# Kernel optimization log

Measured on AMD Instinct MI355X. Metric: run time of the kernel, lower is better.

Reference implementation:

```python
import jax, jax.numpy as jnp
import numpy as np

T, H, E, I, K = 4096, 1024, 16, 768, 8  # tokens, hidden, experts, intermediate, top_k


def setup_inputs() -> dict:
    key = jax.random.key(0)
    k0, k1, k2, k3, k4 = jax.random.split(key, 5)
    scale = 0.02
    return {
        "hidden_states": jax.random.normal(k0, (T, H), dtype=jnp.float32),
        "gate_w": jax.random.normal(k1, (H, E), dtype=jnp.float32) * scale,
        "w1": jax.random.normal(k2, (E, H, I), dtype=jnp.float32) * scale,  # gate proj
        "w3": jax.random.normal(k3, (E, H, I), dtype=jnp.float32) * scale,  # up proj
        "w2": jax.random.normal(k4, (E, I, H), dtype=jnp.float32) * scale,  # down proj
    }


def reference(hidden_states, gate_w, w1, w3, w2):
    x = hidden_states  # [T, H]
    # Router: replicated linear (no bias) -> softmax -> top-k -> renormalize
    router_logits = x @ gate_w  # [T, E]
    probs = jax.nn.softmax(router_logits.astype(jnp.float32), axis=-1)
    topk_w, topk_idx = jax.lax.top_k(probs, K)  # [T, K]
    topk_w = topk_w / jnp.sum(topk_w, axis=-1, keepdims=True)  # norm_topk_prob=True
    # Dense routing-weight matrix [T, E]: zero for non-selected experts
    dense_w = jnp.zeros((T, E), dtype=x.dtype)
    dense_w = dense_w.at[jnp.arange(T)[:, None], topk_idx].set(topk_w.astype(x.dtype))
    # SwiGLU experts, computed densely over experts and masked by routing weights
    h = jnp.einsum("th,ehi->tei", x, w1)  # [T, E, I]
    u = jnp.einsum("th,ehi->tei", x, w3)  # [T, E, I]
    act = jax.nn.silu(h) * u  # [T, E, I]
    out = jnp.einsum("tei,eih,te->th", act, w2, dense_w)  # weighted combine -> [T, H]
    return out
```

## Files before the change

kernel.cpp:

```cpp
#include <hip/hip_runtime.h>
#include <hip/hip_bf16.h>

#define T_ 4096
#define H_ 1024
#define E_ 16
#define I_ 768
#define KTOP 8
#define MAXSLOT 4096
#define ACT_ROWS 34816

typedef __attribute__((ext_vector_type(8))) short bf16x8;
typedef __attribute__((ext_vector_type(4))) float f32x4;

__device__ __forceinline__ unsigned short f2bf(float f) {
  unsigned u = __builtin_bit_cast(unsigned, f);
  u += 0x7fff + ((u >> 16) & 1);
  return (unsigned short)(u >> 16);
}
__device__ __forceinline__ float bf2f(unsigned short u) {
  unsigned v = ((unsigned)u) << 16;
  return __builtin_bit_cast(float, v);
}

typedef __attribute__((address_space(3))) void lds_void;
typedef __attribute__((address_space(1))) void g_void;

__device__ __forceinline__ void gload_lds16(const void* g, void* l) {
  __builtin_amdgcn_global_load_lds((g_void*)g, (lds_void*)l, 16, 0, 0);
}

__global__ void router_kernel(const float* __restrict__ x,
                              const float* __restrict__ gate_w,
                              int* __restrict__ cnt,
                              int* __restrict__ tok_list,
                              float* __restrict__ rw_list,
                              int* __restrict__ tok2es) {
  int t = blockIdx.x;
  int lane = threadIdx.x;
  int e = lane & 15;
  int chunk = lane >> 4;
  const float* xr = x + (size_t)t * H_;
  int h0 = chunk * 256;
  float partial = 0.f;
  for (int i = 0; i < 256; i += 4) {
    float4 xv = *reinterpret_cast<const float4*>(xr + h0 + i);
    partial += xv.x * gate_w[(size_t)(h0 + i    ) * E_ + e];
    partial += xv.y * gate_w[(size_t)(h0 + i + 1) * E_ + e];
    partial += xv.z * gate_w[(size_t)(h0 + i + 2) * E_ + e];
    partial += xv.w * gate_w[(size_t)(h0 + i + 3) * E_ + e];
  }
  partial += __shfl_xor(partial, 16);
  partial += __shfl_xor(partial, 32);
  float logit = partial;
  float m = logit;
  for (int d = 1; d < 16; d <<= 1) m = fmaxf(m, __shfl_xor(m, d));
  float p = __expf(logit - m);
  int base = lane & ~15;
  int rank = 0;
  for (int j = 0; j < 16; ++j) {
    float pj = __shfl(p, base + j);
    rank += (pj > p) || (pj == p && j < e);
  }
  bool sel = rank < KTOP;
  float contrib = sel ? p : 0.f;
  float s = contrib;
  for (int d = 1; d < 16; d <<= 1) s += __shfl_xor(s, d);
  float w = sel ? p / s : 0.f;
  if (lane < 16 && sel) {
    int slot = atomicAdd(&cnt[e], 1);
    tok_list[e * MAXSLOT + slot] = t;
    rw_list[e * MAXSLOT + slot] = w;
    tok2es[t * KTOP + rank] = (e << 20) | slot;
  }
}

__global__ void offsets_kernel(const int* __restrict__ cnt,
                               int* __restrict__ off,
                               int* __restrict__ ntiles) {
  int acc = 0;
  for (int e = 0; e < E_; ++e) {
    off[e] = acc;
    int nt = (cnt[e] + 127) >> 7;
    ntiles[e] = nt;
    acc += nt << 7;
  }
}

__global__ void cast_x_kernel(const float* __restrict__ x,
                              unsigned short* __restrict__ xb) {
  int idx = blockIdx.x * blockDim.x + threadIdx.x;
  float4 v = reinterpret_cast<const float4*>(x)[idx];
  ushort4 o;
  o.x = f2bf(v.x); o.y = f2bf(v.y); o.z = f2bf(v.z); o.w = f2bf(v.w);
  *reinterpret_cast<ushort4*>(xb + (size_t)idx * 4) = o;
}

__global__ void transpose_w13_kernel(const float* __restrict__ w1,
                                     const float* __restrict__ w3,
                                     unsigned short* __restrict__ w1t,
                                     unsigned short* __restrict__ w3t) {
  __shared__ float tile[64][65];
  int i0 = blockIdx.x * 64;
  int h0 = blockIdx.y * 64;
  int e = blockIdx.z & 15;
  const float* src = (blockIdx.z < 16 ? w1 : w3) + (size_t)e * H_ * I_;
  unsigned short* dst = (blockIdx.z < 16 ? w1t : w3t) + (size_t)e * I_ * H_;
  int tx = threadIdx.x & 63, ty = threadIdx.x >> 6;
  for (int r = 0; r < 64; r += 4)
    tile[ty + r][tx] = src[(size_t)(h0 + ty + r) * I_ + i0 + tx];
  __syncthreads();
  for (int r = 0; r < 64; r += 4) {
    int i = ty + r;
    dst[(size_t)(i0 + i) * H_ + h0 + tx] = f2bf(tile[tx][i]);
  }
}

__global__ void transpose_w2_kernel(const float* __restrict__ w2,
                                    unsigned short* __restrict__ w2te) {
  __shared__ float tile[64][65];
  int h0 = blockIdx.x * 64;
  int i0 = blockIdx.y * 64;
  int e = blockIdx.z;
  const float* src = w2 + (size_t)e * I_ * H_;
  int tx = threadIdx.x & 63, ty = threadIdx.x >> 6;
  for (int r = 0; r < 64; r += 4)
    tile[ty + r][tx] = src[(size_t)(i0 + ty + r) * H_ + h0 + tx];
  __syncthreads();
  for (int r = 0; r < 64; r += 4) {
    int h = ty + r;
    w2te[((size_t)e * H_ + h0 + h) * I_ + i0 + tx] = f2bf(tile[tx][h]);
  }
}

__global__ __launch_bounds__(256) void moe_up_kernel(
    const unsigned short* __restrict__ xb,
    const unsigned short* __restrict__ w1t,
    const unsigned short* __restrict__ w3t,
    const int* __restrict__ tok_list,
    const float* __restrict__ rw_list,
    const int* __restrict__ off,
    const int* __restrict__ ntiles,
    unsigned short* __restrict__ act_g) {
  const int e = blockIdx.z;
  const int tile = blockIdx.x;
  if (tile >= ntiles[e]) return;

  __shared__ __align__(16) unsigned short Asm[128 * 32];
  __shared__ __align__(16) unsigned short B1sm[64 * 32];
  __shared__ __align__(16) unsigned short B3sm[64 * 32];
  __shared__ int tok_sm[128];
  __shared__ float rw_sm[128];

  const int col0 = blockIdx.y * 64;
  const int tid = threadIdx.x;
  const int lane = tid & 63;
  const int w = tid >> 6;
  const int wm = w >> 1, wn = w & 1;
  const int slot0 = off[e] + tile * 128;

  if (tid < 128) {
    int li = e * MAXSLOT + tile * 128 + tid;
    tok_sm[tid] = tok_list[li];
    rw_sm[tid] = rw_list[li];
  }
  __syncthreads();

  const int r_in_chunk = lane >> 2;
  const int kpart = (lane & 3) * 8;

  const unsigned short* asrc[4];
  if (w < 2) {
#pragma unroll
    for (int i = 0; i < 4; ++i) {
      int row = (w * 4 + i) * 16 + r_in_chunk;
      asrc[i] = xb + (size_t)tok_sm[row] * H_ + kpart;
    }
  }
  const unsigned short* B1base = w1t + ((size_t)e * I_ + col0) * H_;
  const unsigned short* B3base = w3t + ((size_t)e * I_ + col0) * H_;

  f32x4 acc1[4][2] = {};
  f32x4 acc2[4][2] = {};

  const int lrow = lane & 15;
  const int lk = (lane >> 4) * 8;

  for (int k0 = 0; k0 < H_; k0 += 32) {
    if (w < 2) {
#pragma unroll
      for (int i = 0; i < 4; ++i)
        gload_lds16(asrc[i] + k0, &Asm[(w * 4 + i) * 512]);
    } else if (w == 2) {
#pragma unroll
      for (int i = 0; i < 4; ++i) {
        int row = i * 16 + r_in_chunk;
        gload_lds16(B1base + (size_t)row * H_ + k0 + kpart, &B1sm[i * 512]);
      }
    } else {
#pragma unroll
      for (int i = 0; i < 4; ++i) {
        int row = i * 16 + r_in_chunk;
        gload_lds16(B3base + (size_t)row * H_ + k0 + kpart, &B3sm[i * 512]);
      }
    }
    __syncthreads();
    bf16x8 af[4], b1f[2], b3f[2];
    for (int m = 0; m < 4; ++m)
      af[m] = *reinterpret_cast<const bf16x8*>(&Asm[(wm * 64 + m * 16 + lrow) * 32 + lk]);
    for (int n = 0; n < 2; ++n) {
      b1f[n] = *reinterpret_cast<const bf16x8*>(&B1sm[(wn * 32 + n * 16 + lrow) * 32 + lk]);
      b3f[n] = *reinterpret_cast<const bf16x8*>(&B3sm[(wn * 32 + n * 16 + lrow) * 32 + lk]);
    }
    for (int m = 0; m < 4; ++m)
      for (int n = 0; n < 2; ++n) {
        acc1[m][n] = __builtin_amdgcn_mfma_f32_16x16x32_bf16(af[m], b1f[n], acc1[m][n], 0, 0, 0);
        acc2[m][n] = __builtin_amdgcn_mfma_f32_16x16x32_bf16(af[m], b3f[n], acc2[m][n], 0, 0, 0);
      }
    __syncthreads();
  }

  const int crow = (lane >> 4) * 4;
  const int ccol = lane & 15;
  for (int m = 0; m < 4; ++m)
    for (int n = 0; n < 2; ++n)
      for (int r = 0; r < 4; ++r) {
        int rl = wm * 64 + m * 16 + crow + r;
        int cl = wn * 32 + n * 16 + ccol;
        float hv = acc1[m][n][r];
        float uv = acc2[m][n][r];
        float a = (hv / (1.f + __expf(-hv))) * uv * rw_sm[rl];
        act_g[(size_t)(slot0 + rl) * I_ + col0 + cl] = f2bf(a);
      }
}

__global__ __launch_bounds__(256) void moe_down_kernel(
    const unsigned short* __restrict__ act_g,
    const unsigned short* __restrict__ w2te,
    const int* __restrict__ off,
    const int* __restrict__ ntiles,
    unsigned short* __restrict__ dout_g) {
  const int e = blockIdx.z;
  const int tile = blockIdx.x;
  if (tile >= ntiles[e]) return;

  __shared__ __align__(16) unsigned short Asm[128 * 32];
  __shared__ __align__(16) unsigned short Bsm[128 * 32];

  const int col0 = blockIdx.y * 128;
  const int tid = threadIdx.x;
  const int lane = tid & 63;
  const int w = tid >> 6;
  const int wm = w >> 1, wn = w & 1;
  const int slot0 = off[e] + tile * 128;

  const int r_in_chunk = lane >> 2;
  const int kpart = (lane & 3) * 8;

  const unsigned short* Abase = act_g + (size_t)slot0 * I_;
  const unsigned short* Bbase = w2te + ((size_t)e * H_ + col0) * I_;

  f32x4 acc[4][4] = {};

  const int lrow = lane & 15;
  const int lk = (lane >> 4) * 8;

  for (int k0 = 0; k0 < I_; k0 += 32) {
    for (int i = 0; i < 2; ++i) {
      int c = w * 2 + i;
      int row = c * 16 + r_in_chunk;
      gload_lds16(Abase + (size_t)row * I_ + k0 + kpart, &Asm[c * 512]);
      gload_lds16(Bbase + (size_t)row * I_ + k0 + kpart, &Bsm[c * 512]);
    }
    __syncthreads();
    bf16x8 af[4], bf[4];
    for (int m = 0; m < 4; ++m)
      af[m] = *reinterpret_cast<const bf16x8*>(&Asm[(wm * 64 + m * 16 + lrow) * 32 + lk]);
    for (int n = 0; n < 4; ++n)
      bf[n] = *reinterpret_cast<const bf16x8*>(&Bsm[(wn * 64 + n * 16 + lrow) * 32 + lk]);
    for (int m = 0; m < 4; ++m)
      for (int n = 0; n < 4; ++n)
        acc[m][n] = __builtin_amdgcn_mfma_f32_16x16x32_bf16(af[m], bf[n], acc[m][n], 0, 0, 0);
    __syncthreads();
  }

  const int crow = (lane >> 4) * 4;
  const int ccol = lane & 15;
  for (int m = 0; m < 4; ++m)
    for (int n = 0; n < 4; ++n)
      for (int r = 0; r < 4; ++r) {
        int rl = wm * 64 + m * 16 + crow + r;
        int cl = wn * 64 + n * 16 + ccol;
        dout_g[(size_t)(slot0 + rl) * H_ + col0 + cl] = f2bf(acc[m][n][r]);
      }
}

__global__ __launch_bounds__(256) void combine_kernel(
    const unsigned short* __restrict__ dout_g,
    const int* __restrict__ tok2es,
    const int* __restrict__ off,
    float* __restrict__ out) {
  __shared__ int gs[KTOP];
  int t = blockIdx.x;
  if (threadIdx.x < KTOP) {
    int es = tok2es[t * KTOP + threadIdx.x];
    int e = es >> 20, s = es & 0xFFFFF;
    gs[threadIdx.x] = off[e] + s;
  }
  __syncthreads();
  int h = threadIdx.x * 4;
  float4 sum = {0.f, 0.f, 0.f, 0.f};
#pragma unroll
  for (int k = 0; k < KTOP; ++k) {
    ushort4 v = *reinterpret_cast<const ushort4*>(&dout_g[(size_t)gs[k] * H_ + h]);
    sum.x += bf2f(v.x);
    sum.y += bf2f(v.y);
    sum.z += bf2f(v.z);
    sum.w += bf2f(v.w);
  }
  *reinterpret_cast<float4*>(&out[(size_t)t * H_ + h]) = sum;
}

extern "C" void kernel_launch(void* const* d_in, const int* in_sizes, int n_in,
                              void* d_out, int out_size, void* d_ws, size_t ws_size,
                              hipStream_t stream) {
  const float* x      = (const float*)d_in[0];
  const float* gate_w = (const float*)d_in[1];
  const float* w1     = (const float*)d_in[2];
  const float* w3     = (const float*)d_in[3];
  const float* w2     = (const float*)d_in[4];
  float* out = (float*)d_out;

  char* ws = (char*)d_ws;
  int* ctrl     = (int*)ws;
  int* cnt      = ctrl;
  int* off      = ctrl + 16;
  int* ntiles   = ctrl + 32;
  int* tok_list = ctrl + 64;
  float* rw_list = (float*)(tok_list + E_ * MAXSLOT);
  int* tok2es   = (int*)(rw_list + E_ * MAXSLOT);
  unsigned short* xb    = (unsigned short*)(ws + (1 << 20));
  unsigned short* w2te  = xb + (size_t)T_ * H_;
  unsigned short* act_g = w2te + (size_t)E_ * H_ * I_;
  unsigned short* w1t   = act_g + (size_t)ACT_ROWS * I_;
  unsigned short* w3t   = w1t + (size_t)E_ * I_ * H_;
  unsigned short* dout_g = w1t;

  hipMemsetAsync(d_ws, 0, (64 + 2 * E_ * MAXSLOT + T_ * KTOP) * sizeof(int), stream);

  router_kernel<<<T_, 64, 0, stream>>>(x, gate_w, cnt, tok_list, rw_list, tok2es);
  offsets_kernel<<<1, 1, 0, stream>>>(cnt, off, ntiles);
  cast_x_kernel<<<(T_ * H_ / 4) / 256, 256, 0, stream>>>(x, xb);
  transpose_w13_kernel<<<dim3(I_ / 64, H_ / 64, 32), 256, 0, stream>>>(w1, w3, w1t, w3t);
  transpose_w2_kernel<<<dim3(H_ / 64, I_ / 64, E_), 256, 0, stream>>>(w2, w2te);
  moe_up_kernel<<<dim3(32, I_ / 64, E_), 256, 0, stream>>>(
      xb, w1t, w3t, tok_list, rw_list, off, ntiles, act_g);
  moe_down_kernel<<<dim3(32, H_ / 128, E_), 256, 0, stream>>>(
      act_g, w2te, off, ntiles, dout_g);
  combine_kernel<<<T_, 256, 0, stream>>>(dout_g, tok2es, off, out);
}
```

Before: 620.5 us.

## Enlarge MoE GEMM tiles to 256 rows with 512-thread blocks and K-step 64

The up- and down-projection grouped GEMMs move from 128-row tiles to 256-row tiles. Both kernels now use 8-wave blocks and a K step of 64 instead of 32. In the up kernel each wave computes 64x64 for both the gate and up projections, and in the down kernel each wave computes 128x64. Expert padding and the activation buffer grow to 256-row granularity to match. The aim is more MFMA work per LDS load and per barrier, and better operand reuse. In exchange it raises register and LDS pressure (64KB per block), adds padding waste per expert, and leaves fewer blocks to spread across CUs.

```diff
diff --git a/kernel.cpp b/kernel.cpp
--- a/kernel.cpp
+++ b/kernel.cpp
@@ -7,7 +7,7 @@
 #define I_ 768
 #define KTOP 8
 #define MAXSLOT 4096
-#define ACT_ROWS 34816
+#define ACT_ROWS 36864
 
 typedef __attribute__((ext_vector_type(8))) short bf16x8;
 typedef __attribute__((ext_vector_type(4))) float f32x4;
@@ -80,9 +80,9 @@
   int acc = 0;
   for (int e = 0; e < E_; ++e) {
     off[e] = acc;
-    int nt = (cnt[e] + 127) >> 7;
+    int nt = (cnt[e] + 255) >> 8;
     ntiles[e] = nt;
-    acc += nt << 7;
+    acc += nt << 8;
   }
 }
 
@@ -132,7 +132,7 @@
   }
 }
 
-__global__ __launch_bounds__(256) void moe_up_kernel(
+__global__ __launch_bounds__(512, 2) void moe_up_kernel(
     const unsigned short* __restrict__ xb,
     const unsigned short* __restrict__ w1t,
     const unsigned short* __restrict__ w3t,
@@ -145,87 +145,99 @@
   const int tile = blockIdx.x;
   if (tile >= ntiles[e]) return;
 
-  __shared__ __align__(16) unsigned short Asm[128 * 32];
-  __shared__ __align__(16) unsigned short B1sm[64 * 32];
-  __shared__ __align__(16) unsigned short B3sm[64 * 32];
-  __shared__ int tok_sm[128];
-  __shared__ float rw_sm[128];
-
-  const int col0 = blockIdx.y * 64;
+  __shared__ __align__(16) unsigned short Asm[256 * 64];
+  __shared__ __align__(16) unsigned short B1sm[128 * 64];
+  __shared__ __align__(16) unsigned short B3sm[128 * 64];
+  __shared__ int tok_sm[256];
+  __shared__ float rw_sm[256];
+
+  const int col0 = blockIdx.y * 128;
   const int tid = threadIdx.x;
   const int lane = tid & 63;
   const int w = tid >> 6;
   const int wm = w >> 1, wn = w & 1;
-  const int slot0 = off[e] + tile * 128;
-
-  if (tid < 128) {
-    int li = e * MAXSLOT + tile * 128 + tid;
+  const int slot0 = off[e] + tile * 256;
+
+  if (tid < 256) {
+    int li = e * MAXSLOT + tile * 256 + tid;
     tok_sm[tid] = tok_list[li];
     rw_sm[tid] = rw_list[li];
   }
   __syncthreads();
 
-  const int r_in_chunk = lane >> 2;
-  const int kpart = (lane & 3) * 8;
-
-  const unsigned short* asrc[4];
-  if (w < 2) {
-#pragma unroll
-    for (int i = 0; i < 4; ++i) {
-      int row = (w * 4 + i) * 16 + r_in_chunk;
-      asrc[i] = xb + (size_t)tok_sm[row] * H_ + kpart;
-    }
-  }
-  const unsigned short* B1base = w1t + ((size_t)e * I_ + col0) * H_;
-  const unsigned short* B3base = w3t + ((size_t)e * I_ + col0) * H_;
-
-  f32x4 acc1[4][2] = {};
-  f32x4 acc2[4][2] = {};
+  const int lr = lane >> 3;
+  const int lc = (lane & 7) * 8;
+
+  const unsigned short* src[8];
+  unsigned short* ldst[8];
+  if (w < 4) {
+#pragma unroll
+    for (int c = 0; c < 8; ++c) {
+      int row = w * 64 + c * 8 + lr;
+      src[c] = xb + (size_t)tok_sm[row] * H_ + lc;
+      ldst[c] = &Asm[(w * 8 + c) * 512];
+    }
+  } else if (w < 6) {
+#pragma unroll
+    for (int c = 0; c < 8; ++c) {
+      int j = (w - 4) * 64 + c * 8 + lr;
+      src[c] = w1t + ((size_t)e * I_ + col0 + j) * H_ + lc;
+      ldst[c] = &B1sm[((w - 4) * 8 + c) * 512];
+    }
+  } else {
+#pragma unroll
+    for (int c = 0; c < 8; ++c) {
+      int j = (w - 6) * 64 + c * 8 + lr;
+      src[c] = w3t + ((size_t)e * I_ + col0 + j) * H_ + lc;
+      ldst[c] = &B3sm[((w - 6) * 8 + c) * 512];
+    }
+  }
+
+  f32x4 acc1[4][4] = {};
+  f32x4 acc2[4][4] = {};
 
   const int lrow = lane & 15;
-  const int lk = (lane >> 4) * 8;
-
-  for (int k0 = 0; k0 < H_; k0 += 32) {
-    if (w < 2) {
-#pragma unroll
-      for (int i = 0; i < 4; ++i)
-        gload_lds16(asrc[i] + k0, &Asm[(w * 4 + i) * 512]);
-    } else if (w == 2) {
-#pragma unroll
-      for (int i = 0; i < 4; ++i) {
-        int row = i * 16 + r_in_chunk;
-        gload_lds16(B1base + (size_t)row * H_ + k0 + kpart, &B1sm[i * 512]);
+  const int lk8 = (lane >> 4) * 8;
+
+  for (int k0 = 0; k0 < H_; k0 += 64) {
+#pragma unroll
+    for (int c = 0; c < 8; ++c) gload_lds16(src[c] + k0, ldst[c]);
+    __syncthreads();
+#pragma unroll
+    for (int kk = 0; kk < 2; ++kk) {
+      bf16x8 a[4], b1[4], b3[4];
+#pragma unroll
+      for (int m = 0; m < 4; ++m)
+        a[m] = *reinterpret_cast<const bf16x8*>(
+            &Asm[(wm * 64 + m * 16 + lrow) * 64 + kk * 32 + lk8]);
+#pragma unroll
+      for (int n = 0; n < 4; ++n) {
+        b1[n] = *reinterpret_cast<const bf16x8*>(
+            &B1sm[(wn * 64 + n * 16 + lrow) * 64 + kk * 32 + lk8]);
+        b3[n] = *reinterpret_cast<const bf16x8*>(
+            &B3sm[(wn * 64 + n * 16 + lrow) * 64 + kk * 32 + lk8]);
       }
-    } else {
-#pragma unroll
-      for (int i = 0; i < 4; ++i) {
-        int row = i * 16 + r_in_chunk;
-        gload_lds16(B3base + (size_t)row * H_ + k0 + kpart, &B3sm[i * 512]);
-      }
-    }
-    __syncthreads();
-    bf16x8 af[4], b1f[2], b3f[2];
-    for (int m = 0; m < 4; ++m)
-      af[m] = *reinterpret_cast<const bf16x8*>(&Asm[(wm * 64 + m * 16 + lrow) * 32 + lk]);
-    for (int n = 0; n < 2; ++n) {
-      b1f[n] = *reinterpret_cast<const bf16x8*>(&B1sm[(wn * 32 + n * 16 + lrow) * 32 + lk]);
-      b3f[n] = *reinterpret_cast<const bf16x8*>(&B3sm[(wn * 32 + n * 16 + lrow) * 32 + lk]);
-    }
-    for (int m = 0; m < 4; ++m)
-      for (int n = 0; n < 2; ++n) {
-        acc1[m][n] = __builtin_amdgcn_mfma_f32_16x16x32_bf16(af[m], b1f[n], acc1[m][n], 0, 0, 0);
-        acc2[m][n] = __builtin_amdgcn_mfma_f32_16x16x32_bf16(af[m], b3f[n], acc2[m][n], 0, 0, 0);
-      }
+#pragma unroll
+      for (int m = 0; m < 4; ++m)
+#pragma unroll
+        for (int n = 0; n < 4; ++n) {
+          acc1[m][n] = __builtin_amdgcn_mfma_f32_16x16x32_bf16(a[m], b1[n], acc1[m][n], 0, 0, 0);
+          acc2[m][n] = __builtin_amdgcn_mfma_f32_16x16x32_bf16(a[m], b3[n], acc2[m][n], 0, 0, 0);
+        }
+    }
     __syncthreads();
   }
 
   const int crow = (lane >> 4) * 4;
   const int ccol = lane & 15;
+#pragma unroll
   for (int m = 0; m < 4; ++m)
-    for (int n = 0; n < 2; ++n)
+#pragma unroll
+    for (int n = 0; n < 4; ++n)
+#pragma unroll
       for (int r = 0; r < 4; ++r) {
         int rl = wm * 64 + m * 16 + crow + r;
-        int cl = wn * 32 + n * 16 + ccol;
+        int cl = wn * 64 + n * 16 + ccol;
         float hv = acc1[m][n][r];
         float uv = acc2[m][n][r];
         float a = (hv / (1.f + __expf(-hv))) * uv * rw_sm[rl];
@@ -233,7 +245,7 @@
       }
 }
 
-__global__ __launch_bounds__(256) void moe_down_kernel(
+__global__ __launch_bounds__(512, 2) void moe_down_kernel(
     const unsigned short* __restrict__ act_g,
     const unsigned short* __restrict__ w2te,
     const int* __restrict__ off,
@@ -243,52 +255,75 @@
   const int tile = blockIdx.x;
   if (tile >= ntiles[e]) return;
 
-  __shared__ __align__(16) unsigned short Asm[128 * 32];
-  __shared__ __align__(16) unsigned short Bsm[128 * 32];
-
-  const int col0 = blockIdx.y * 128;
+  __shared__ __align__(16) unsigned short Asm[256 * 64];
+  __shared__ __align__(16) unsigned short Bsm[256 * 64];
+
+  const int col0 = blockIdx.y * 256;
   const int tid = threadIdx.x;
   const int lane = tid & 63;
   const int w = tid >> 6;
-  const int wm = w >> 1, wn = w & 1;
-  const int slot0 = off[e] + tile * 128;
-
-  const int r_in_chunk = lane >> 2;
-  const int kpart = (lane & 3) * 8;
-
-  const unsigned short* Abase = act_g + (size_t)slot0 * I_;
-  const unsigned short* Bbase = w2te + ((size_t)e * H_ + col0) * I_;
-
-  f32x4 acc[4][4] = {};
+  const int wm = w >> 2, wn = w & 3;
+  const int slot0 = off[e] + tile * 256;
+
+  const int lr = lane >> 3;
+  const int lc = (lane & 7) * 8;
+
+  const unsigned short* src[8];
+  unsigned short* ldst[8];
+  if (w < 4) {
+#pragma unroll
+    for (int c = 0; c < 8; ++c) {
+      int row = w * 64 + c * 8 + lr;
+      src[c] = act_g + (size_t)(slot0 + row) * I_ + lc;
+      ldst[c] = &Asm[(w * 8 + c) * 512];
+    }
+  } else {
+#pragma unroll
+    for (int c = 0; c < 8; ++c) {
+      int j = (w - 4) * 64 + c * 8 + lr;
+      src[c] = w2te + ((size_t)e * H_ + col0 + j) * I_ + lc;
+      ldst[c] = &Bsm[((w - 4) * 8 + c) * 512];
+    }
+  }
+
+  f32x4 acc[8][4] = {};
 
   const int lrow = lane & 15;
-  const int lk = (lane >> 4) * 8;
-
-  for (int k0 = 0; k0 < I_; k0 += 32) {
-    for (int i = 0; i < 2; ++i) {
-      int c = w * 2 + i;
-      int row = c * 16 + r_in_chunk;
-      gload_lds16(Abase + (size_t)row * I_ + k0 + kpart, &Asm[c * 512]);
-      gload_lds16(Bbase + (size_t)row * I_ + k0 + kpart, &Bsm[c * 512]);
-    }
+  const int lk8 = (lane >> 4) * 8;
+
+  for (int k0 = 0; k0 < I_; k0 += 64) {
+#pragma unroll
+    for (int c = 0; c < 8; ++c) gload_lds16(src[c] + k0, ldst[c]);
     __syncthreads();
-    bf16x8 af[4], bf[4];
-    for (int m = 0; m < 4; ++m)
-      af[m] = *reinterpret_cast<const bf16x8*>(&Asm[(wm * 64 + m * 16 + lrow) * 32 + lk]);
-    for (int n = 0; n < 4; ++n)
-      bf[n] = *reinterpret_cast<const bf16x8*>(&Bsm[(wn * 64 + n * 16 + lrow) * 32 + lk]);
-    for (int m = 0; m < 4; ++m)
+#pragma unroll
+    for (int kk = 0; kk < 2; ++kk) {
+      bf16x8 a[8], b[4];
+#pragma unroll
+      for (int m = 0; m < 8; ++m)
+        a[m] = *reinterpret_cast<const bf16x8*>(
+            &Asm[(wm * 128 + m * 16 + lrow) * 64 + kk * 32 + lk8]);
+#pragma unroll
       for (int n = 0; n < 4; ++n)
-        acc[m][n] = __builtin_amdgcn_mfma_f32_16x16x32_bf16(af[m], bf[n], acc[m][n], 0, 0, 0);
+        b[n] = *reinterpret_cast<const bf16x8*>(
+            &Bsm[(wn * 64 + n * 16 + lrow) * 64 + kk * 32 + lk8]);
+#pragma unroll
+      for (int m = 0; m < 8; ++m)
+#pragma unroll
+        for (int n = 0; n < 4; ++n)
+          acc[m][n] = __builtin_amdgcn_mfma_f32_16x16x32_bf16(a[m], b[n], acc[m][n], 0, 0, 0);
+    }
     __syncthreads();
   }
 
   const int crow = (lane >> 4) * 4;
   const int ccol = lane & 15;
-  for (int m = 0; m < 4; ++m)
+#pragma unroll
+  for (int m = 0; m < 8; ++m)
+#pragma unroll
     for (int n = 0; n < 4; ++n)
+#pragma unroll
       for (int r = 0; r < 4; ++r) {
-        int rl = wm * 64 + m * 16 + crow + r;
+        int rl = wm * 128 + m * 16 + crow + r;
         int cl = wn * 64 + n * 16 + ccol;
         dout_g[(size_t)(slot0 + rl) * H_ + col0 + cl] = f2bf(acc[m][n][r]);
       }
@@ -352,9 +387,9 @@
   cast_x_kernel<<<(T_ * H_ / 4) / 256, 256, 0, stream>>>(x, xb);
   transpose_w13_kernel<<<dim3(I_ / 64, H_ / 64, 32), 256, 0, stream>>>(w1, w3, w1t, w3t);
   transpose_w2_kernel<<<dim3(H_ / 64, I_ / 64, E_), 256, 0, stream>>>(w2, w2te);
-  moe_up_kernel<<<dim3(32, I_ / 64, E_), 256, 0, stream>>>(
+  moe_up_kernel<<<dim3(16, I_ / 128, E_), 512, 0, stream>>>(
       xb, w1t, w3t, tok_list, rw_list, off, ntiles, act_g);
-  moe_down_kernel<<<dim3(32, H_ / 128, E_), 256, 0, stream>>>(
+  moe_down_kernel<<<dim3(16, H_ / 256, E_), 512, 0, stream>>>(
       act_g, w2te, off, ntiles, dout_g);
   combine_kernel<<<T_, 256, 0, stream>>>(dout_g, tok2es, off, out);
 }
```

Measured after the change: 679.2 us. 1.09x slower.
